# Performance work log

Hardware: AMD Instinct MI355X
Metric: run time of the kernel (lower is better)

Reference implementation:

```python
import jax, jax.numpy as jnp
import numpy as np

B = 4           # batchsize == poolsize, pool = arange(B)
N_NODES = 32768
N_EDGES = 262144
CH_V = 16
CH_E = 16
HID = 64
CH_MSG = 2 * CH_V + CH_E  # 48


def setup_inputs() -> dict:
    key = jax.random.key(0)
    ks = jax.random.split(key, 8)
    node_vals = jax.random.normal(ks[0], (B, N_NODES, CH_V), jnp.float32) * 0.01
    edge_vals = jax.random.normal(ks[1], (B, N_EDGES, CH_E), jnp.float32) * 0.1
    conn_a = jax.random.randint(ks[2], (N_EDGES,), 0, N_NODES)
    conn_b = jax.random.randint(ks[3], (N_EDGES,), 0, N_NODES)
    w = lambda k, sh: jax.random.normal(k, sh, jnp.float32) * 0.1
    return {
        "node_vals": node_vals, "edge_vals": edge_vals,
        "conn_a": conn_a, "conn_b": conn_b,
        "Wm1": w(ks[4], (CH_MSG, HID)), "bm1": jnp.zeros((HID,), jnp.float32),
        "Wm2": w(ks[5], (HID, CH_MSG)), "bm2": jnp.zeros((CH_MSG,), jnp.float32),
        "Wu1": w(ks[6], (3 * CH_V, HID)), "bu1": jnp.zeros((HID,), jnp.float32),
        "Wu2": w(ks[7], (HID, CH_V)), "bu2": jnp.zeros((CH_V,), jnp.float32),
    }


def reference(node_vals, edge_vals, conn_a, conn_b,
              Wm1, bm1, Wm2, bm2, Wu1, bu1, Wu2, bu2):
    # NeuralGraph.timestep with node_dropout_p = edge_dropout_p = 0 (masks are identity),
    # use_update=True, average_messages=True, nodes=True, edges=True.
    h_a = node_vals[:, conn_a]                      # [B, E, CH_V] gather at source nodes
    h_b = node_vals[:, conn_b]                      # [B, E, CH_V] gather at target nodes
    h = jnp.concatenate([h_a, h_b, edge_vals], -1)  # [B, E, 48]
    # message MLP (Linear -> tanh -> Linear)
    m = jnp.tanh(h @ Wm1 + bm1) @ Wm2 + bm2         # [B, E, 48]
    m_a = m[..., :CH_V]
    m_b = m[..., CH_V:2 * CH_V]
    m_ab = m[..., 2 * CH_V:]
    # scatter-add aggregation per node (index_add_ along node dim)
    agg_a = jnp.zeros((B, N_NODES, CH_V), m.dtype).at[:, conn_a].add(m_a)
    agg_b = jnp.zeros((B, N_NODES, CH_V), m.dtype).at[:, conn_b].add(m_b)
    # count-based averaging (counts clamped to >= 1, matching the buffer fixup)
    ones = jnp.ones((N_EDGES,), m.dtype)
    cnt_a = jnp.maximum(jax.ops.segment_sum(ones, conn_a, num_segments=N_NODES), 1.0)
    cnt_b = jnp.maximum(jax.ops.segment_sum(ones, conn_b, num_segments=N_NODES), 1.0)
    agg_a = agg_a / cnt_a[None, :, None]
    agg_b = agg_b / cnt_b[None, :, None]
    # update MLP
    u_in = jnp.concatenate([agg_a, agg_b, node_vals], -1)   # [B, N, 48]
    updates = jnp.tanh(u_in @ Wu1 + bu1) @ Wu2 + bu2        # [B, N, CH_V]
    new_node_vals = node_vals + updates
    new_edge_vals = edge_vals + m_ab
    return new_node_vals, new_edge_vals
```

## Files before the change

### kernel.cpp

```cpp
#include <hip/hip_runtime.h>
#include <hip/hip_bf16.h>
#include <cstdint>
#include <cstddef>

#define B 4
#define NN 32768
#define NE 262144
#define CV 16
#define CE 16
#define HID 64
#define CM 48
#define HS 72

using frag  = __attribute__((ext_vector_type(8))) short;
using f32x4 = __attribute__((ext_vector_type(4))) float;

__device__ __forceinline__ float fast_tanh(float x) {
    float e = __expf(2.0f * x);
    return 1.0f - 2.0f / (e + 1.0f);
}

__device__ __forceinline__ unsigned short f2bf(float x) {
    union { float f; unsigned u; } v; v.f = x;
    unsigned r = (v.u + 0x7FFFu + ((v.u >> 16) & 1u)) >> 16;
    return (unsigned short)r;
}

__device__ __forceinline__ float bf2f(unsigned short x) {
    union { unsigned u; float f; } v; v.u = ((unsigned)x) << 16;
    return v.f;
}

__device__ __forceinline__ unsigned pk2bf(float lo, float hi) {
    union { __hip_bfloat162 h; unsigned u; } v;
    v.h = __float22bfloat162_rn(make_float2(lo, hi));
    return v.u;
}

__global__ __launch_bounds__(256) void count_kernel(
    const int* __restrict__ ca, const int* __restrict__ cb,
    int* __restrict__ cnt_a, int* __restrict__ cnt_b,
    int* __restrict__ rank_a, int* __restrict__ rank_b,
    const float* __restrict__ Wm1, const float* __restrict__ bm1,
    const float* __restrict__ Wm2,
    unsigned short* __restrict__ pW1, unsigned short* __restrict__ pW2)
{
    int i = blockIdx.x * 256 + threadIdx.x;
    rank_a[i] = atomicAdd(&cnt_a[ca[i]], 1);
    rank_b[i] = atomicAdd(&cnt_b[cb[i]], 1);

    if (blockIdx.x == 0) {
        for (int x = threadIdx.x; x < 4 * 2 * 64 * 8; x += 256) {
            int j = x & 7, lane = (x >> 3) & 63, ks = (x >> 9) & 1, mt = x >> 10;
            int m = mt * 16 + (lane & 15);
            int k = ks * 32 + (lane >> 4) * 8 + j;
            float w = (k < 48) ? Wm1[k * 64 + m] : (k == 48 ? bm1[m] : 0.0f);
            pW1[x] = f2bf(w);
        }
    } else if (blockIdx.x == 1) {
        for (int x = threadIdx.x; x < 3 * 2 * 64 * 8; x += 256) {
            int j = x & 7, lane = (x >> 3) & 63, ks = (x >> 9) & 1, mt = x >> 10;
            int m = mt * 16 + (lane & 15);
            int k = ks * 32 + (lane >> 4) * 8 + j;
            pW2[x] = f2bf(Wm2[k * 48 + m]);
        }
    }
}

__global__ __launch_bounds__(1024) void scan_kernel(
    const int* __restrict__ cnt_a, int* __restrict__ start_a,
    const int* __restrict__ cnt_b, int* __restrict__ start_b)
{
    const int* cnt = (blockIdx.x == 0) ? cnt_a : cnt_b;
    int* start     = (blockIdx.x == 0) ? start_a : start_b;

    __shared__ int s[1024];
    int t = threadIdx.x;
    int base = t * 32;
    int local[32];
    int sum = 0;
#pragma unroll
    for (int i = 0; i < 32; i++) { local[i] = cnt[base + i]; sum += local[i]; }
    s[t] = sum;
    __syncthreads();
    for (int off = 1; off < 1024; off <<= 1) {
        int add = (t >= off) ? s[t - off] : 0;
        __syncthreads();
        s[t] += add;
        __syncthreads();
    }
    int run = s[t] - sum;
#pragma unroll
    for (int i = 0; i < 32; i++) {
        start[base + i] = run;
        run += local[i];
    }
}

__global__ __launch_bounds__(256) void edge_kernel(
    const float* __restrict__ node_vals, const float* __restrict__ edge_vals,
    const int* __restrict__ ca, const int* __restrict__ cb,
    const int* __restrict__ rank_a, const int* __restrict__ rank_b,
    const int* __restrict__ start_a, const int* __restrict__ start_b,
    const unsigned short* __restrict__ pW1, const unsigned short* __restrict__ pW2,
    const float* __restrict__ bm2,
    float* __restrict__ out_edge,
    unsigned short* __restrict__ ma_csr, unsigned short* __restrict__ mb_csr)
{
    __shared__ unsigned short sH[256 * HS];
    __shared__ float sb2f[CM];

    int t = threadIdx.x;
    int lane = t & 63;
    int wv   = t >> 6;
    int col  = lane & 15;
    int quad = lane >> 4;
    int erow = wv * 64;
    int cha  = quad * 4;

    frag w1f[4][2];
#pragma unroll
    for (int mt = 0; mt < 4; mt++)
#pragma unroll
        for (int ks = 0; ks < 2; ks++)
            w1f[mt][ks] = *(const frag*)&pW1[(((mt * 2 + ks) * 64) + lane) * 8];

    if (t < CM) sb2f[t] = bm2[t];

    size_t eb = (size_t)blockIdx.x * 256;
    int posx, posy;
    {
        size_t idx = eb + t;
        int e = (int)(idx & (NE - 1));
        int bb = (int)(idx >> 18);
        int na = ca[e], nb = cb[e];
        posx = start_a[na] + rank_a[e];
        posy = start_b[nb] + rank_b[e];
        float h[48];
        const float4* pA = (const float4*)(node_vals + ((size_t)bb * NN + na) * CV);
        const float4* pB = (const float4*)(node_vals + ((size_t)bb * NN + nb) * CV);
        const float4* pE = (const float4*)(edge_vals + idx * CE);
#pragma unroll
        for (int q = 0; q < 4; q++) {
            float4 va = pA[q];
            h[q*4+0] = va.x; h[q*4+1] = va.y; h[q*4+2] = va.z; h[q*4+3] = va.w;
            float4 vb = pB[q];
            h[16+q*4+0] = vb.x; h[16+q*4+1] = vb.y; h[16+q*4+2] = vb.z; h[16+q*4+3] = vb.w;
            float4 ve = pE[q];
            h[32+q*4+0] = ve.x; h[32+q*4+1] = ve.y; h[32+q*4+2] = ve.z; h[32+q*4+3] = ve.w;
        }
        unsigned pk[32];
#pragma unroll
        for (int q = 0; q < 24; q++) pk[q] = pk2bf(h[2*q], h[2*q+1]);
        pk[24] = 0x3F80u;
#pragma unroll
        for (int q = 25; q < 32; q++) pk[q] = 0;
        uint4* row = (uint4*)&sH[t * HS];
        const uint4* src = (const uint4*)pk;
#pragma unroll
        for (int q = 0; q < 8; q++) row[q] = src[q];
    }
    __syncthreads();

    f32x4 acc1[4][4];
#pragma unroll
    for (int mt = 0; mt < 4; mt++)
#pragma unroll
        for (int nt = 0; nt < 4; nt++) acc1[mt][nt] = (f32x4){0.f, 0.f, 0.f, 0.f};

#pragma unroll
    for (int ks = 0; ks < 2; ks++) {
        frag bfr[4];
#pragma unroll
        for (int nt = 0; nt < 4; nt++)
            bfr[nt] = *(const frag*)&sH[(erow + nt*16 + col) * HS + ks*32 + quad*8];
#pragma unroll
        for (int mt = 0; mt < 4; mt++)
#pragma unroll
            for (int nt = 0; nt < 4; nt++)
                acc1[mt][nt] = __builtin_amdgcn_mfma_f32_16x16x32_bf16(w1f[mt][ks], bfr[nt], acc1[mt][nt], 0, 0, 0);
    }

    __syncthreads();

    frag w2f[3][2];
#pragma unroll
    for (int mt = 0; mt < 3; mt++)
#pragma unroll
        for (int ks = 0; ks < 2; ks++)
            w2f[mt][ks] = *(const frag*)&pW2[(((mt * 2 + ks) * 64) + lane) * 8];

#pragma unroll
    for (int nt = 0; nt < 4; nt++) {
        int row = erow + nt*16 + col;
#pragma unroll
        for (int mt = 0; mt < 4; mt++) {
            uint2 w;
            w.x = pk2bf(fast_tanh(acc1[mt][nt][0]), fast_tanh(acc1[mt][nt][1]));
            w.y = pk2bf(fast_tanh(acc1[mt][nt][2]), fast_tanh(acc1[mt][nt][3]));
            *(uint2*)&sH[row * HS + mt*16 + quad*4] = w;
        }
    }
    __syncthreads();

    f32x4 acc2[3][4];
#pragma unroll
    for (int mt = 0; mt < 3; mt++)
#pragma unroll
        for (int nt = 0; nt < 4; nt++) acc2[mt][nt] = (f32x4){0.f, 0.f, 0.f, 0.f};

#pragma unroll
    for (int ks = 0; ks < 2; ks++) {
        frag bfr[4];
#pragma unroll
        for (int nt = 0; nt < 4; nt++)
            bfr[nt] = *(const frag*)&sH[(erow + nt*16 + col) * HS + ks*32 + quad*8];
#pragma unroll
        for (int mt = 0; mt < 3; mt++)
#pragma unroll
            for (int nt = 0; nt < 4; nt++)
                acc2[mt][nt] = __builtin_amdgcn_mfma_f32_16x16x32_bf16(w2f[mt][ks], bfr[nt], acc2[mt][nt], 0, 0, 0);
    }

#pragma unroll
    for (int nt = 0; nt < 4; nt++) {
        int le = erow + nt*16 + col;
        size_t o = (eb + le) * CE + cha;
        float4 ev = *(const float4*)&edge_vals[o];
        float4 ov;
        ov.x = ev.x + acc2[2][nt][0] + sb2f[32+cha+0];
        ov.y = ev.y + acc2[2][nt][1] + sb2f[32+cha+1];
        ov.z = ev.z + acc2[2][nt][2] + sb2f[32+cha+2];
        ov.w = ev.w + acc2[2][nt][3] + sb2f[32+cha+3];
        *(float4*)&out_edge[o] = ov;
    }

    __syncthreads();

#pragma unroll
    for (int nt = 0; nt < 4; nt++) {
        int row = erow + nt*16 + col;
        uint2 wa;
        wa.x = pk2bf(acc2[0][nt][0] + sb2f[cha+0], acc2[0][nt][1] + sb2f[cha+1]);
        wa.y = pk2bf(acc2[0][nt][2] + sb2f[cha+2], acc2[0][nt][3] + sb2f[cha+3]);
        *(uint2*)&sH[row * HS + cha] = wa;
        uint2 wb;
        wb.x = pk2bf(acc2[1][nt][0] + sb2f[16+cha+0], acc2[1][nt][1] + sb2f[16+cha+1]);
        wb.y = pk2bf(acc2[1][nt][2] + sb2f[16+cha+2], acc2[1][nt][3] + sb2f[16+cha+3]);
        *(uint2*)&sH[row * HS + 16 + cha] = wb;
    }
    __syncthreads();

    {
        int bb = (int)((eb + t) >> 18);
        uint4 a0 = *(const uint4*)&sH[t * HS + 0];
        uint4 a1 = *(const uint4*)&sH[t * HS + 8];
        uint4 b0 = *(const uint4*)&sH[t * HS + 16];
        uint4 b1 = *(const uint4*)&sH[t * HS + 24];
        unsigned short* pa = &ma_csr[((size_t)bb * NE + posx) * 16];
        *(uint4*)(pa + 0) = a0;
        *(uint4*)(pa + 8) = a1;
        unsigned short* pb = &mb_csr[((size_t)bb * NE + posy) * 16];
        *(uint4*)(pb + 0) = b0;
        *(uint4*)(pb + 8) = b1;
    }
}

__global__ __launch_bounds__(256) void agg_kernel(
    const unsigned short* __restrict__ ma_csr, const unsigned short* __restrict__ mb_csr,
    const int* __restrict__ start_a, const int* __restrict__ start_b,
    const int* __restrict__ cnt_a, const int* __restrict__ cnt_b,
    float* __restrict__ agg_a, float* __restrict__ agg_b)
{
    int t = threadIdx.x;
    int team = t >> 5;
    int half = (t >> 4) & 1;
    int l16  = t & 15;
    int eoff  = l16 >> 1;
    int chunk = l16 & 1;
    int g = blockIdx.x * 8 + team;
    int n = g & (NN - 1);
    int b = g >> 15;

    const unsigned short* mcsr = half ? mb_csr : ma_csr;
    const int* stp  = half ? start_b : start_a;
    const int* cntp = half ? cnt_b   : cnt_a;
    float* aggp     = half ? agg_b   : agg_a;

    int d = cntp[n];
    int s = stp[n];
    const unsigned short* base = mcsr + ((size_t)b * NE + s) * 16 + chunk * 8;

    float acc[8] = {0.f, 0.f, 0.f, 0.f, 0.f, 0.f, 0.f, 0.f};
    for (int k = eoff; k < d; k += 8) {
        uint4 v = *(const uint4*)(base + (size_t)k * 16);
        acc[0] += bf2f((unsigned short)(v.x & 0xFFFFu));
        acc[1] += bf2f((unsigned short)(v.x >> 16));
        acc[2] += bf2f((unsigned short)(v.y & 0xFFFFu));
        acc[3] += bf2f((unsigned short)(v.y >> 16));
        acc[4] += bf2f((unsigned short)(v.z & 0xFFFFu));
        acc[5] += bf2f((unsigned short)(v.z >> 16));
        acc[6] += bf2f((unsigned short)(v.w & 0xFFFFu));
        acc[7] += bf2f((unsigned short)(v.w >> 16));
    }
#pragma unroll
    for (int m = 2; m <= 8; m <<= 1) {
#pragma unroll
        for (int i = 0; i < 8; i++) acc[i] += __shfl_xor(acc[i], m);
    }

    if (eoff == 0) {
        float inv = 1.0f / (float)max(d, 1);
        float4 r0, r1;
        r0.x = acc[0]*inv; r0.y = acc[1]*inv; r0.z = acc[2]*inv; r0.w = acc[3]*inv;
        r1.x = acc[4]*inv; r1.y = acc[5]*inv; r1.z = acc[6]*inv; r1.w = acc[7]*inv;
        float* dst = &aggp[(size_t)g * CV + chunk * 8];
        *(float4*)(dst + 0) = r0;
        *(float4*)(dst + 4) = r1;
    }
}

__global__ __launch_bounds__(256) void node_kernel(
    const float* __restrict__ node_vals,
    const float* __restrict__ agg_a, const float* __restrict__ agg_b,
    const float* __restrict__ Wu1, const float* __restrict__ bu1,
    const float* __restrict__ Wu2, const float* __restrict__ bu2,
    float* __restrict__ out_node)
{
    __shared__ float sW1[HID * CM];
    __shared__ float sW2[HID * CV];
    __shared__ float sb1[HID];
    __shared__ float sb2[CV];

    int t = threadIdx.x;
    for (int x = t; x < HID * CM; x += 256) {
        int k = x / CM, i = x - k * CM;
        sW1[x] = Wu1[i * HID + k];
    }
    for (int x = t; x < HID * CV; x += 256) sW2[x] = Wu2[x];
    if (t < HID) sb1[t] = bu1[t];
    if (t < CV)  sb2[t] = bu2[t];
    __syncthreads();

    int idx = blockIdx.x * 256 + t;

    float u[CM];
    const float4* pa = (const float4*)(agg_a + (size_t)idx * CV);
    const float4* pb = (const float4*)(agg_b + (size_t)idx * CV);
    const float4* pn = (const float4*)(node_vals + (size_t)idx * CV);
#pragma unroll
    for (int q = 0; q < 4; q++) {
        float4 va = pa[q];
        u[q*4+0] = va.x; u[q*4+1] = va.y; u[q*4+2] = va.z; u[q*4+3] = va.w;
        float4 vb = pb[q];
        u[16+q*4+0] = vb.x; u[16+q*4+1] = vb.y; u[16+q*4+2] = vb.z; u[16+q*4+3] = vb.w;
        float4 vn = pn[q];
        u[32+q*4+0] = vn.x; u[32+q*4+1] = vn.y; u[32+q*4+2] = vn.z; u[32+q*4+3] = vn.w;
    }

    float o[CV];
#pragma unroll
    for (int j = 0; j < CV; j++) o[j] = sb2[j];

    for (int k = 0; k < HID; k++) {
        float acc = sb1[k];
        const float* w1 = &sW1[k * CM];
#pragma unroll
        for (int i = 0; i < CM; i++) acc = fmaf(u[i], w1[i], acc);
        float th = fast_tanh(acc);
        const float* w2 = &sW2[k * CV];
#pragma unroll
        for (int j = 0; j < CV; j++) o[j] = fmaf(th, w2[j], o[j]);
    }

    float4* on = (float4*)(out_node + (size_t)idx * CV);
#pragma unroll
    for (int q = 0; q < 4; q++) {
        on[q] = make_float4(u[32+q*4+0] + o[q*4+0],
                            u[32+q*4+1] + o[q*4+1],
                            u[32+q*4+2] + o[q*4+2],
                            u[32+q*4+3] + o[q*4+3]);
    }
}

extern "C" void kernel_launch(void* const* d_in, const int* in_sizes, int n_in,
                              void* d_out, int out_size, void* d_ws, size_t ws_size,
                              hipStream_t stream) {
    const float* node_vals = (const float*)d_in[0];
    const float* edge_vals = (const float*)d_in[1];
    const int*   ca        = (const int*)d_in[2];
    const int*   cb        = (const int*)d_in[3];
    const float* Wm1 = (const float*)d_in[4];
    const float* bm1 = (const float*)d_in[5];
    const float* Wm2 = (const float*)d_in[6];
    const float* bm2 = (const float*)d_in[7];
    const float* Wu1 = (const float*)d_in[8];
    const float* bu1 = (const float*)d_in[9];
    const float* Wu2 = (const float*)d_in[10];
    const float* bu2 = (const float*)d_in[11];

    float* out_node = (float*)d_out;
    float* out_edge = out_node + (size_t)B * NN * CV;

    unsigned short* ma_csr = (unsigned short*)d_ws;
    unsigned short* mb_csr = ma_csr + (size_t)B * NE * 16;
    float* agg_a = (float*)(mb_csr + (size_t)B * NE * 16);
    float* agg_b = agg_a + (size_t)B * NN * CV;
    int* cnt_a   = (int*)(agg_b + (size_t)B * NN * CV);
    int* cnt_b   = cnt_a + NN;
    int* start_a = cnt_b + NN;
    int* start_b = start_a + NN;
    int* rank_a  = start_b + NN;
    int* rank_b  = rank_a + NE;
    unsigned short* pW1 = (unsigned short*)(rank_b + NE);
    unsigned short* pW2 = pW1 + 4096;

    hipMemsetAsync(cnt_a, 0, 2 * (size_t)NN * sizeof(int), stream);

    count_kernel<<<NE / 256, 256, 0, stream>>>(
        ca, cb, cnt_a, cnt_b, rank_a, rank_b, Wm1, bm1, Wm2, pW1, pW2);
    scan_kernel<<<2, 1024, 0, stream>>>(cnt_a, start_a, cnt_b, start_b);
    edge_kernel<<<(B * NE) / 256, 256, 0, stream>>>(
        node_vals, edge_vals, ca, cb, rank_a, rank_b, start_a, start_b,
        pW1, pW2, bm2, out_edge, ma_csr, mb_csr);
    agg_kernel<<<(B * NN) / 8, 256, 0, stream>>>(
        ma_csr, mb_csr, start_a, start_b, cnt_a, cnt_b, agg_a, agg_b);
    node_kernel<<<(B * NN) / 256, 256, 0, stream>>>(
        node_vals, agg_a, agg_b, Wu1, bu1, Wu2, bu2, out_node);
}
```

Baseline: 322.8 us.

## Rework edge kernel into per-wave halves with swizzled LDS and warp-shuffle scan

The edge MLP kernel now processes each wave's 64 edges in two 32-row halves. This shrinks the accumulator register arrays, and a launch bound asks for 5 blocks per CU to raise occupancy. The padded LDS row stride is replaced by an XOR-swizzled 128-byte layout. Block-wide __syncthreads are replaced by s_waitcnt, since each wave only touches its own rows. Bias values are read straight from global memory, and the scan kernel switches from a shared-memory Hillis-Steele loop to wave shuffles with vectorised loads and stores. This relies on wave-private LDS rows being correct without barriers, and weights are reloaded once per half.

```diff
diff --git a/kernel.cpp b/kernel.cpp
--- a/kernel.cpp
+++ b/kernel.cpp
@@ -10,7 +10,6 @@
 #define CE 16
 #define HID 64
 #define CM 48
-#define HS 72
 
 using frag  = __attribute__((ext_vector_type(8))) short;
 using f32x4 = __attribute__((ext_vector_type(4))) float;
@@ -35,6 +34,10 @@
     union { __hip_bfloat162 h; unsigned u; } v;
     v.h = __float22bfloat162_rn(make_float2(lo, hi));
     return v.u;
+}
+
+__device__ __forceinline__ unsigned swo(int row, int byte_off) {
+    return (unsigned)((row << 7) + (byte_off ^ ((row & 7) << 4)));
 }
 
 __global__ __launch_bounds__(256) void count_kernel(
@@ -74,30 +77,55 @@
     const int* cnt = (blockIdx.x == 0) ? cnt_a : cnt_b;
     int* start     = (blockIdx.x == 0) ? start_a : start_b;
 
-    __shared__ int s[1024];
+    __shared__ int sw[16];
     int t = threadIdx.x;
+    int lane = t & 63;
+    int wv   = t >> 6;
     int base = t * 32;
+
     int local[32];
     int sum = 0;
-#pragma unroll
-    for (int i = 0; i < 32; i++) { local[i] = cnt[base + i]; sum += local[i]; }
-    s[t] = sum;
+    const int4* p = (const int4*)(cnt + base);
+#pragma unroll
+    for (int q = 0; q < 8; q++) {
+        int4 v = p[q];
+        local[q*4+0] = v.x; local[q*4+1] = v.y; local[q*4+2] = v.z; local[q*4+3] = v.w;
+        sum += v.x + v.y + v.z + v.w;
+    }
+    int inc = sum;
+#pragma unroll
+    for (int off = 1; off < 64; off <<= 1) {
+        int u = __shfl_up(inc, off);
+        if (lane >= off) inc += u;
+    }
+    if (lane == 63) sw[wv] = inc;
     __syncthreads();
-    for (int off = 1; off < 1024; off <<= 1) {
-        int add = (t >= off) ? s[t - off] : 0;
-        __syncthreads();
-        s[t] += add;
-        __syncthreads();
-    }
-    int run = s[t] - sum;
-#pragma unroll
-    for (int i = 0; i < 32; i++) {
-        start[base + i] = run;
-        run += local[i];
-    }
-}
-
-__global__ __launch_bounds__(256) void edge_kernel(
+    if (wv == 0 && lane < 16) {
+        int v = sw[lane];
+        int i2 = v;
+#pragma unroll
+        for (int off = 1; off < 16; off <<= 1) {
+            int u = __shfl_up(i2, off);
+            if (lane >= off) i2 += u;
+        }
+        sw[lane] = i2 - v;
+    }
+    __syncthreads();
+
+    int run = sw[wv] + inc - sum;
+    int4* ps = (int4*)(start + base);
+#pragma unroll
+    for (int q = 0; q < 8; q++) {
+        int4 o;
+        o.x = run; run += local[q*4+0];
+        o.y = run; run += local[q*4+1];
+        o.z = run; run += local[q*4+2];
+        o.w = run; run += local[q*4+3];
+        ps[q] = o;
+    }
+}
+
+__global__ __launch_bounds__(256, 5) void edge_kernel(
     const float* __restrict__ node_vals, const float* __restrict__ edge_vals,
     const int* __restrict__ ca, const int* __restrict__ cb,
     const int* __restrict__ rank_a, const int* __restrict__ rank_b,
@@ -107,31 +135,21 @@
     float* __restrict__ out_edge,
     unsigned short* __restrict__ ma_csr, unsigned short* __restrict__ mb_csr)
 {
-    __shared__ unsigned short sH[256 * HS];
-    __shared__ float sb2f[CM];
-
-    int t = threadIdx.x;
+    __shared__ unsigned short sH[256 * 64];
+    char* sB = (char*)sH;
+
+    int t    = threadIdx.x;
     int lane = t & 63;
-    int wv   = t >> 6;
     int col  = lane & 15;
     int quad = lane >> 4;
-    int erow = wv * 64;
+    int erow = (t >> 6) * 64;
     int cha  = quad * 4;
-
-    frag w1f[4][2];
-#pragma unroll
-    for (int mt = 0; mt < 4; mt++)
-#pragma unroll
-        for (int ks = 0; ks < 2; ks++)
-            w1f[mt][ks] = *(const frag*)&pW1[(((mt * 2 + ks) * 64) + lane) * 8];
-
-    if (t < CM) sb2f[t] = bm2[t];
 
     size_t eb = (size_t)blockIdx.x * 256;
     int posx, posy;
     {
         size_t idx = eb + t;
-        int e = (int)(idx & (NE - 1));
+        int e  = (int)(idx & (NE - 1));
         int bb = (int)(idx >> 18);
         int na = ca[e], nb = cb[e];
         posx = start_a[na] + rank_a[e];
@@ -155,108 +173,121 @@
         pk[24] = 0x3F80u;
 #pragma unroll
         for (int q = 25; q < 32; q++) pk[q] = 0;
-        uint4* row = (uint4*)&sH[t * HS];
         const uint4* src = (const uint4*)pk;
 #pragma unroll
-        for (int q = 0; q < 8; q++) row[q] = src[q];
-    }
-    __syncthreads();
-
-    f32x4 acc1[4][4];
-#pragma unroll
-    for (int mt = 0; mt < 4; mt++)
-#pragma unroll
-        for (int nt = 0; nt < 4; nt++) acc1[mt][nt] = (f32x4){0.f, 0.f, 0.f, 0.f};
-
-#pragma unroll
-    for (int ks = 0; ks < 2; ks++) {
-        frag bfr[4];
-#pragma unroll
-        for (int nt = 0; nt < 4; nt++)
-            bfr[nt] = *(const frag*)&sH[(erow + nt*16 + col) * HS + ks*32 + quad*8];
+        for (int q = 0; q < 8; q++)
+            *(uint4*)(sB + swo(t, q * 16)) = src[q];
+    }
+    asm volatile("s_waitcnt lgkmcnt(0)" ::: "memory");
+
+#pragma unroll
+    for (int hh = 0; hh < 2; hh++) {
+        int r0 = erow + hh * 32 + col;
+
+        frag w1f[4][2];
 #pragma unroll
         for (int mt = 0; mt < 4; mt++)
 #pragma unroll
-            for (int nt = 0; nt < 4; nt++)
-                acc1[mt][nt] = __builtin_amdgcn_mfma_f32_16x16x32_bf16(w1f[mt][ks], bfr[nt], acc1[mt][nt], 0, 0, 0);
-    }
-
-    __syncthreads();
-
-    frag w2f[3][2];
-#pragma unroll
-    for (int mt = 0; mt < 3; mt++)
-#pragma unroll
-        for (int ks = 0; ks < 2; ks++)
-            w2f[mt][ks] = *(const frag*)&pW2[(((mt * 2 + ks) * 64) + lane) * 8];
-
-#pragma unroll
-    for (int nt = 0; nt < 4; nt++) {
-        int row = erow + nt*16 + col;
-#pragma unroll
-        for (int mt = 0; mt < 4; mt++) {
-            uint2 w;
-            w.x = pk2bf(fast_tanh(acc1[mt][nt][0]), fast_tanh(acc1[mt][nt][1]));
-            w.y = pk2bf(fast_tanh(acc1[mt][nt][2]), fast_tanh(acc1[mt][nt][3]));
-            *(uint2*)&sH[row * HS + mt*16 + quad*4] = w;
-        }
-    }
-    __syncthreads();
-
-    f32x4 acc2[3][4];
-#pragma unroll
-    for (int mt = 0; mt < 3; mt++)
-#pragma unroll
-        for (int nt = 0; nt < 4; nt++) acc2[mt][nt] = (f32x4){0.f, 0.f, 0.f, 0.f};
-
-#pragma unroll
-    for (int ks = 0; ks < 2; ks++) {
-        frag bfr[4];
-#pragma unroll
-        for (int nt = 0; nt < 4; nt++)
-            bfr[nt] = *(const frag*)&sH[(erow + nt*16 + col) * HS + ks*32 + quad*8];
+            for (int ks = 0; ks < 2; ks++)
+                w1f[mt][ks] = *(const frag*)&pW1[(((mt * 2 + ks) * 64) + lane) * 8];
+
+        f32x4 acc1[4][2];
+#pragma unroll
+        for (int mt = 0; mt < 4; mt++)
+#pragma unroll
+            for (int n = 0; n < 2; n++) acc1[mt][n] = (f32x4){0.f, 0.f, 0.f, 0.f};
+
+#pragma unroll
+        for (int ks = 0; ks < 2; ks++) {
+            frag bfr[2];
+#pragma unroll
+            for (int n = 0; n < 2; n++)
+                bfr[n] = *(const frag*)(sB + swo(r0 + n * 16, ks * 64 + quad * 16));
+#pragma unroll
+            for (int mt = 0; mt < 4; mt++)
+#pragma unroll
+                for (int n = 0; n < 2; n++)
+                    acc1[mt][n] = __builtin_amdgcn_mfma_f32_16x16x32_bf16(
+                        w1f[mt][ks], bfr[n], acc1[mt][n], 0, 0, 0);
+        }
+
+#pragma unroll
+        for (int n = 0; n < 2; n++) {
+            int row = r0 + n * 16;
+#pragma unroll
+            for (int mt = 0; mt < 4; mt++) {
+                uint2 w;
+                w.x = pk2bf(fast_tanh(acc1[mt][n][0]), fast_tanh(acc1[mt][n][1]));
+                w.y = pk2bf(fast_tanh(acc1[mt][n][2]), fast_tanh(acc1[mt][n][3]));
+                *(uint2*)(sB + swo(row, mt * 32 + quad * 8)) = w;
+            }
+        }
+        asm volatile("s_waitcnt lgkmcnt(0)" ::: "memory");
+
+        frag w2f[3][2];
 #pragma unroll
         for (int mt = 0; mt < 3; mt++)
 #pragma unroll
-            for (int nt = 0; nt < 4; nt++)
-                acc2[mt][nt] = __builtin_amdgcn_mfma_f32_16x16x32_bf16(w2f[mt][ks], bfr[nt], acc2[mt][nt], 0, 0, 0);
-    }
-
-#pragma unroll
-    for (int nt = 0; nt < 4; nt++) {
-        int le = erow + nt*16 + col;
-        size_t o = (eb + le) * CE + cha;
-        float4 ev = *(const float4*)&edge_vals[o];
-        float4 ov;
-        ov.x = ev.x + acc2[2][nt][0] + sb2f[32+cha+0];
-        ov.y = ev.y + acc2[2][nt][1] + sb2f[32+cha+1];
-        ov.z = ev.z + acc2[2][nt][2] + sb2f[32+cha+2];
-        ov.w = ev.w + acc2[2][nt][3] + sb2f[32+cha+3];
-        *(float4*)&out_edge[o] = ov;
-    }
-
-    __syncthreads();
-
-#pragma unroll
-    for (int nt = 0; nt < 4; nt++) {
-        int row = erow + nt*16 + col;
-        uint2 wa;
-        wa.x = pk2bf(acc2[0][nt][0] + sb2f[cha+0], acc2[0][nt][1] + sb2f[cha+1]);
-        wa.y = pk2bf(acc2[0][nt][2] + sb2f[cha+2], acc2[0][nt][3] + sb2f[cha+3]);
-        *(uint2*)&sH[row * HS + cha] = wa;
-        uint2 wb;
-        wb.x = pk2bf(acc2[1][nt][0] + sb2f[16+cha+0], acc2[1][nt][1] + sb2f[16+cha+1]);
-        wb.y = pk2bf(acc2[1][nt][2] + sb2f[16+cha+2], acc2[1][nt][3] + sb2f[16+cha+3]);
-        *(uint2*)&sH[row * HS + 16 + cha] = wb;
-    }
-    __syncthreads();
+            for (int ks = 0; ks < 2; ks++)
+                w2f[mt][ks] = *(const frag*)&pW2[(((mt * 2 + ks) * 64) + lane) * 8];
+
+        f32x4 acc2[3][2];
+#pragma unroll
+        for (int mt = 0; mt < 3; mt++)
+#pragma unroll
+            for (int n = 0; n < 2; n++) acc2[mt][n] = (f32x4){0.f, 0.f, 0.f, 0.f};
+
+#pragma unroll
+        for (int ks = 0; ks < 2; ks++) {
+            frag bfr[2];
+#pragma unroll
+            for (int n = 0; n < 2; n++)
+                bfr[n] = *(const frag*)(sB + swo(r0 + n * 16, ks * 64 + quad * 16));
+#pragma unroll
+            for (int mt = 0; mt < 3; mt++)
+#pragma unroll
+                for (int n = 0; n < 2; n++)
+                    acc2[mt][n] = __builtin_amdgcn_mfma_f32_16x16x32_bf16(
+                        w2f[mt][ks], bfr[n], acc2[mt][n], 0, 0, 0);
+        }
+
+        float4 b2e = *(const float4*)&bm2[32 + cha];
+#pragma unroll
+        for (int n = 0; n < 2; n++) {
+            int le = r0 + n * 16;
+            size_t o = (eb + le) * CE + cha;
+            float4 ev = *(const float4*)&edge_vals[o];
+            float4 ov;
+            ov.x = ev.x + acc2[2][n][0] + b2e.x;
+            ov.y = ev.y + acc2[2][n][1] + b2e.y;
+            ov.z = ev.z + acc2[2][n][2] + b2e.z;
+            ov.w = ev.w + acc2[2][n][3] + b2e.w;
+            *(float4*)&out_edge[o] = ov;
+        }
+
+        float4 b2a = *(const float4*)&bm2[cha];
+        float4 b2b = *(const float4*)&bm2[16 + cha];
+#pragma unroll
+        for (int n = 0; n < 2; n++) {
+            int row = r0 + n * 16;
+            uint2 wa;
+            wa.x = pk2bf(acc2[0][n][0] + b2a.x, acc2[0][n][1] + b2a.y);
+            wa.y = pk2bf(acc2[0][n][2] + b2a.z, acc2[0][n][3] + b2a.w);
+            *(uint2*)(sB + swo(row, quad * 8)) = wa;
+            uint2 wb;
+            wb.x = pk2bf(acc2[1][n][0] + b2b.x, acc2[1][n][1] + b2b.y);
+            wb.y = pk2bf(acc2[1][n][2] + b2b.z, acc2[1][n][3] + b2b.w);
+            *(uint2*)(sB + swo(row, 32 + quad * 8)) = wb;
+        }
+    }
+    asm volatile("s_waitcnt lgkmcnt(0)" ::: "memory");
 
     {
         int bb = (int)((eb + t) >> 18);
-        uint4 a0 = *(const uint4*)&sH[t * HS + 0];
-        uint4 a1 = *(const uint4*)&sH[t * HS + 8];
-        uint4 b0 = *(const uint4*)&sH[t * HS + 16];
-        uint4 b1 = *(const uint4*)&sH[t * HS + 24];
+        uint4 a0 = *(const uint4*)(sB + swo(t, 0));
+        uint4 a1 = *(const uint4*)(sB + swo(t, 16));
+        uint4 b0 = *(const uint4*)(sB + swo(t, 32));
+        uint4 b1 = *(const uint4*)(sB + swo(t, 48));
         unsigned short* pa = &ma_csr[((size_t)bb * NE + posx) * 16];
         *(uint4*)(pa + 0) = a0;
         *(uint4*)(pa + 8) = a1;
```

Measured after the change: 341.8 us. 5.9% more time.
